# Performance work log

Measured on AMD Instinct MI355X. Metric: run time of the kernel, lower is better.

Reference implementation:

```python
import jax, jax.numpy as jnp
import numpy as np

D_MODEL = 1024
NUM_HEADS = 16
D_FF = 4096
BATCH = 4
SEQ = 1024
EPS = 1e-5
ROPE_THETA = 10000.0


def trunc_normal(key, shape):
    # approximate torch trunc_normal_(mean=0, std=1, a=-2, b=2)
    return jax.random.truncated_normal(key, -2.0, 2.0, shape, dtype=jnp.float32)


def setup_inputs() -> dict:
    key = jax.random.key(0)
    ks = jax.random.split(key, 10)
    d, h, f = D_MODEL, NUM_HEADS, D_FF
    return {
        "x": jax.random.normal(ks[0], (BATCH, SEQ, d), dtype=jnp.float32),
        "wq": trunc_normal(ks[1], (d, d)),
        "wk": trunc_normal(ks[2], (d, d)),
        "wv": trunc_normal(ks[3], (d, d)),
        "wo": trunc_normal(ks[4], (d, d)),
        "w1": trunc_normal(ks[5], (f, d)),
        "w2": trunc_normal(ks[6], (d, f)),
        "w3": trunc_normal(ks[7], (f, d)),
        "g1": trunc_normal(ks[8], (d,)),
        "g2": trunc_normal(ks[9], (d,)),
    }


def rms_norm(x, g):
    # source sums (x^2 + eps) then divides by d -> mean(x^2) + eps
    rms = jnp.sqrt(jnp.mean(jnp.square(x), axis=-1, keepdims=True) + EPS)
    return x * g / rms


def apply_rope(x, pos):
    # x: [b, h, s, d_k]; interleaved-pair rotation, theta=ROPE_THETA
    dk = x.shape[-1]
    inv_freq = ROPE_THETA ** (-jnp.arange(0, dk, 2, dtype=jnp.float32) / dk)
    ang = pos[:, None].astype(jnp.float32) * inv_freq[None, :]  # [s, dk/2]
    cos, sin = jnp.cos(ang), jnp.sin(ang)
    x1, x2 = x[..., 0::2], x[..., 1::2]
    r1 = x1 * cos - x2 * sin
    r2 = x1 * sin + x2 * cos
    return jnp.stack([r1, r2], axis=-1).reshape(x.shape)


def reference(x, wq, wk, wv, wo, w1, w2, w3, g1, g2):
    b, s, d = x.shape
    h, dk = NUM_HEADS, d // NUM_HEADS
    pos = jnp.arange(s)

    # --- attention sub-block (pre-norm) ---
    y = rms_norm(x, g1)
    q = (y @ wq.T).reshape(b, s, h, dk).transpose(0, 2, 1, 3)
    k = (y @ wk.T).reshape(b, s, h, dk).transpose(0, 2, 1, 3)
    v = (y @ wv.T).reshape(b, s, h, dk).transpose(0, 2, 1, 3)
    q = apply_rope(q, pos)
    k = apply_rope(k, pos)
    scores = jnp.einsum('bhqd,bhkd->bhqk', q, k) / jnp.sqrt(jnp.float32(dk))
    causal = jnp.tril(jnp.ones((s, s), dtype=bool))
    scores = jnp.where(causal, scores, -jnp.inf)
    attn = jax.nn.softmax(scores, axis=-1)
    ctx = jnp.einsum('bhqk,bhkd->bhqd', attn, v)
    ctx = ctx.transpose(0, 2, 1, 3).reshape(b, s, d)
    x = x + ctx @ wo.T

    # --- SwiGLU FFN sub-block (pre-norm) ---
    y = rms_norm(x, g2)
    l1 = y @ w1.T
    glu = (jax.nn.sigmoid(l1) * l1) * (y @ w3.T)
    return x + glu @ w2.T
```

## Files before the change

### kernel.cpp

```cpp
#include <hip/hip_runtime.h>

typedef __bf16 bf16;
typedef __attribute__((ext_vector_type(8))) __bf16 bf16x8;
typedef __attribute__((ext_vector_type(4))) float f32x4;

static __device__ __forceinline__ int swz4(int r) { return (r >> 1) & 3; }

static __device__ __forceinline__ void async_cp16(void* lds, const void* g) {
  __builtin_amdgcn_global_load_lds((__attribute__((address_space(1))) void*)g,
                                   (__attribute__((address_space(3))) void*)lds,
                                   16, 0, 0);
}

static __device__ __forceinline__ f32x4 mfma16(bf16x8 a, bf16x8 b, f32x4 c) {
  return __builtin_amdgcn_mfma_f32_16x16x32_bf16(a, b, c, 0, 0, 0);
}

static __device__ __forceinline__ unsigned short bfbits(float f) {
  bf16 b = (bf16)f;
  return __builtin_bit_cast(unsigned short, b);
}

extern "C" __global__ void prep_kernel(
    const float* __restrict__ wq, const float* __restrict__ wk,
    const float* __restrict__ wv, const float* __restrict__ wo,
    const float* __restrict__ w1, const float* __restrict__ w3,
    const float* __restrict__ w2,
    unsigned short* __restrict__ WQH, unsigned short* __restrict__ WQL,
    unsigned short* __restrict__ WKH, unsigned short* __restrict__ WKL,
    unsigned short* __restrict__ WVH, unsigned short* __restrict__ WOH,
    unsigned short* __restrict__ W1H, unsigned short* __restrict__ W3H,
    unsigned short* __restrict__ W2H, float2* __restrict__ rope) {
  const int seg = blockIdx.y;
  const int i = blockIdx.x * 256 + threadIdx.x;
  if (seg == 7) {
    if (i >= 32768) return;
    int s = i >> 5, fi = i & 31;
    float inv_freq = powf(10000.0f, -(2.0f * (float)fi) / 64.0f);
    float ang = (float)s * inv_freq;
    float2 cs;
    cs.x = cosf(ang);
    cs.y = sinf(ang);
    rope[i] = cs;
    return;
  }
  const float* src;
  unsigned short* hi_;
  unsigned short* lo_ = nullptr;
  int n4;
  switch (seg) {
    case 0: src = wq; hi_ = WQH; lo_ = WQL; n4 = 262144; break;
    case 1: src = wk; hi_ = WKH; lo_ = WKL; n4 = 262144; break;
    case 2: src = wv; hi_ = WVH; n4 = 262144; break;
    case 3: src = wo; hi_ = WOH; n4 = 262144; break;
    case 4: src = w1; hi_ = W1H; n4 = 1048576; break;
    case 5: src = w3; hi_ = W3H; n4 = 1048576; break;
    default: src = w2; hi_ = W2H; n4 = 1048576; break;
  }
  if (i >= n4) return;
  float4 v = ((const float4*)src)[i];
  bf16 b0 = (bf16)v.x, b1 = (bf16)v.y, b2 = (bf16)v.z, b3 = (bf16)v.w;
  ushort4 oh;
  oh.x = __builtin_bit_cast(unsigned short, b0);
  oh.y = __builtin_bit_cast(unsigned short, b1);
  oh.z = __builtin_bit_cast(unsigned short, b2);
  oh.w = __builtin_bit_cast(unsigned short, b3);
  ((ushort4*)hi_)[i] = oh;
  if (lo_) {
    ushort4 ol;
    ol.x = bfbits(v.x - (float)b0);
    ol.y = bfbits(v.y - (float)b1);
    ol.z = bfbits(v.z - (float)b2);
    ol.w = bfbits(v.w - (float)b3);
    ((ushort4*)lo_)[i] = ol;
  }
}

extern "C" __global__ __launch_bounds__(256) void rmsnorm_kernel(
    const float* __restrict__ x, const float* __restrict__ g,
    unsigned short* __restrict__ yhi, unsigned short* __restrict__ ylo) {
  int row = blockIdx.x;
  int t = threadIdx.x;
  const float4 xv = *(const float4*)(x + (size_t)row * 1024 + t * 4);
  float ss = xv.x * xv.x + xv.y * xv.y + xv.z * xv.z + xv.w * xv.w;
#pragma unroll
  for (int d = 1; d < 64; d <<= 1) ss += __shfl_xor(ss, d, 64);
  __shared__ float red[4];
  if ((t & 63) == 0) red[t >> 6] = ss;
  __syncthreads();
  float tot = red[0] + red[1] + red[2] + red[3];
  float inv = 1.0f / sqrtf(tot * (1.0f / 1024.0f) + 1e-5f);
  const float4 gv = *(const float4*)(g + t * 4);
  float y0 = xv.x * gv.x * inv, y1 = xv.y * gv.y * inv;
  float y2 = xv.z * gv.z * inv, y3 = xv.w * gv.w * inv;
  bf16 b0 = (bf16)y0, b1 = (bf16)y1, b2 = (bf16)y2, b3 = (bf16)y3;
  ushort4 oh;
  oh.x = __builtin_bit_cast(unsigned short, b0);
  oh.y = __builtin_bit_cast(unsigned short, b1);
  oh.z = __builtin_bit_cast(unsigned short, b2);
  oh.w = __builtin_bit_cast(unsigned short, b3);
  ((ushort4*)yhi)[(size_t)row * 256 + t] = oh;
  if (ylo) {
    ushort4 ol;
    ol.x = bfbits(y0 - (float)b0);
    ol.y = bfbits(y1 - (float)b1);
    ol.z = bfbits(y2 - (float)b2);
    ol.w = bfbits(y3 - (float)b3);
    ((ushort4*)ylo)[(size_t)row * 256 + t] = ol;
  }
}

template <int EPI>
__global__ __launch_bounds__(256, 2) void gemm_nt(
    const bf16* __restrict__ A, const bf16* __restrict__ B, int N, int K, int ldk,
    float* __restrict__ outF, bf16* __restrict__ outB,
    const float* __restrict__ resF) {
  const int bid = blockIdx.x;
  const int xcd = bid & 7, sq = bid >> 3;
  const int z = sq >> 5;
  const int rem = sq & 31;
  const size_t tm = (size_t)(xcd * 4 + (rem >> 3)) * 128;
  const size_t tn = (size_t)(rem & 7) * 128;
  A += (size_t)z * K;
  B += (size_t)z * K;
  __shared__ alignas(16) bf16 As[128 * 64];
  __shared__ alignas(16) bf16 Bs[128 * 64];
  const int tid = threadIdx.x;
  const int lane = tid & 63, wave = tid >> 6;
  const int lo = lane & 15, hi = lane >> 4;
  const int wm = wave >> 1, wn = wave & 1;
  f32x4 acc[4][4] = {};
  for (int k0 = 0; k0 < K; k0 += 64) {
    __syncthreads();
#pragma unroll
    for (int i4 = 0; i4 < 4; i4++) {
      int p = tid + 256 * i4;
      int row = p >> 3, c = p & 7;
      int cs = c ^ (row & 7);
      async_cp16((char*)As + (size_t)p * 16, A + (tm + row) * (size_t)ldk + k0 + cs * 8);
      async_cp16((char*)Bs + (size_t)p * 16, B + (tn + row) * (size_t)ldk + k0 + cs * 8);
    }
    __syncthreads();
#pragma unroll
    for (int kh = 0; kh < 2; kh++) {
      bf16x8 fa[4], fb[4];
#pragma unroll
      for (int i = 0; i < 4; i++) {
        int ra = wm * 64 + i * 16 + lo;
        fa[i] = *(const bf16x8*)((const char*)As + ra * 128 + (((kh * 4 + hi) ^ (ra & 7)) << 4));
        int rb = wn * 64 + i * 16 + lo;
        fb[i] = *(const bf16x8*)((const char*)Bs + rb * 128 + (((kh * 4 + hi) ^ (rb & 7)) << 4));
      }
      __builtin_amdgcn_s_setprio(1);
#pragma unroll
      for (int i = 0; i < 4; i++)
#pragma unroll
        for (int j = 0; j < 4; j++) acc[i][j] = mfma16(fa[i], fb[j], acc[i][j]);
      __builtin_amdgcn_s_setprio(0);
    }
  }
#pragma unroll
  for (int i = 0; i < 4; i++)
#pragma unroll
    for (int j = 0; j < 4; j++)
#pragma unroll
      for (int r = 0; r < 4; r++) {
        size_t m = tm + wm * 64 + i * 16 + hi * 4 + r;
        size_t n = tn + wn * 64 + j * 16 + lo;
        float v = acc[i][j][r];
        if constexpr (EPI == 1) {
          size_t idx = m * (size_t)N + n;
          outF[idx] = v + resF[idx];
        } else {
          atomicAdd(&outF[m * (size_t)N + n], v);
        }
      }
}

extern "C" __global__ __launch_bounds__(256, 2) void gemm_up_kernel(
    const bf16* __restrict__ A, const bf16* __restrict__ B1,
    const bf16* __restrict__ B3, bf16* __restrict__ G) {
  const int bid = blockIdx.x;
  const int xcd = bid & 7, sq = bid >> 3;
  const size_t tm = (size_t)(xcd * 4 + (sq & 3)) * 128;
  const size_t tn = (size_t)(sq >> 2) * 128;
  __shared__ alignas(16) bf16 As[128 * 64];
  __shared__ alignas(16) bf16 B1s[128 * 64];
  __shared__ alignas(16) bf16 B3s[128 * 64];
  const int tid = threadIdx.x;
  const int lane = tid & 63, wave = tid >> 6;
  const int lo = lane & 15, hi = lane >> 4;
  const int wm = wave >> 1, wn = wave & 1;
  f32x4 acc1[4][4] = {}, acc3[4][4] = {};
  for (int k0 = 0; k0 < 1024; k0 += 64) {
    __syncthreads();
#pragma unroll
    for (int i4 = 0; i4 < 4; i4++) {
      int p = tid + 256 * i4;
      int row = p >> 3, c = p & 7;
      int cs = c ^ (row & 7);
      async_cp16((char*)As + (size_t)p * 16, A + (tm + row) * (size_t)1024 + k0 + cs * 8);
      async_cp16((char*)B1s + (size_t)p * 16, B1 + (tn + row) * (size_t)1024 + k0 + cs * 8);
      async_cp16((char*)B3s + (size_t)p * 16, B3 + (tn + row) * (size_t)1024 + k0 + cs * 8);
    }
    __syncthreads();
#pragma unroll
    for (int kh = 0; kh < 2; kh++) {
      bf16x8 fa[4], fb[4];
#pragma unroll
      for (int i = 0; i < 4; i++) {
        int ra = wm * 64 + i * 16 + lo;
        fa[i] = *(const bf16x8*)((const char*)As + ra * 128 + (((kh * 4 + hi) ^ (ra & 7)) << 4));
        int rb = wn * 64 + i * 16 + lo;
        fb[i] = *(const bf16x8*)((const char*)B1s + rb * 128 + (((kh * 4 + hi) ^ (rb & 7)) << 4));
      }
      __builtin_amdgcn_s_setprio(1);
#pragma unroll
      for (int i = 0; i < 4; i++)
#pragma unroll
        for (int j = 0; j < 4; j++) acc1[i][j] = mfma16(fa[i], fb[j], acc1[i][j]);
      __builtin_amdgcn_s_setprio(0);
#pragma unroll
      for (int j = 0; j < 4; j++) {
        int rb = wn * 64 + j * 16 + lo;
        fb[j] = *(const bf16x8*)((const char*)B3s + rb * 128 + (((kh * 4 + hi) ^ (rb & 7)) << 4));
      }
      __builtin_amdgcn_s_setprio(1);
#pragma unroll
      for (int i = 0; i < 4; i++)
#pragma unroll
        for (int j = 0; j < 4; j++) acc3[i][j] = mfma16(fa[i], fb[j], acc3[i][j]);
      __builtin_amdgcn_s_setprio(0);
    }
  }
#pragma unroll
  for (int i = 0; i < 4; i++)
#pragma unroll
    for (int j = 0; j < 4; j++)
#pragma unroll
      for (int r = 0; r < 4; r++) {
        size_t m = tm + wm * 64 + i * 16 + hi * 4 + r;
        size_t n = tn + wn * 64 + j * 16 + lo;
        float v1 = acc1[i][j][r], v3 = acc3[i][j][r];
        G[m * 4096 + n] = (bf16)(v1 / (1.0f + __expf(-v1)) * v3);
      }
}

extern "C" __global__ __launch_bounds__(256, 2) void gemm_qkv_kernel(
    const bf16* __restrict__ Ah, const bf16* __restrict__ Al,
    const bf16* __restrict__ BhQ, const bf16* __restrict__ BlQ,
    const bf16* __restrict__ BhK, const bf16* __restrict__ BlK,
    const bf16* __restrict__ BV,
    const float2* __restrict__ rope,
    bf16* __restrict__ OhQ, bf16* __restrict__ OlQ,
    bf16* __restrict__ OhK, bf16* __restrict__ OlK,
    bf16* __restrict__ Vt) {
  const int bid = blockIdx.x;
  const int xcd = bid & 7, sq = bid >> 3;
  const int z = sq >> 5;
  const int rem = sq & 31;
  const size_t tm = (size_t)(xcd * 4 + (rem >> 3)) * 128;
  const size_t tn = (size_t)(rem & 7) * 128;
  const bf16* Bh = (z == 0) ? BhQ : (z == 1) ? BhK : BV;
  const bf16* Bl = (z == 1) ? BlK : BlQ;
  __shared__ alignas(16) bf16 Ahs[128 * 64], Als[128 * 64];
  __shared__ alignas(16) bf16 Bhs[128 * 64], Bls[128 * 64];
  const int tid = threadIdx.x;
  const int lane = tid & 63, wave = tid >> 6;
  const int lo = lane & 15, hi = lane >> 4;
  const int wm = wave >> 1, wn = wave & 1;
  const int K = 1024;
  f32x4 acc[4][4] = {};
  for (int k0 = 0; k0 < K; k0 += 64) {
    __syncthreads();
#pragma unroll
    for (int i4 = 0; i4 < 4; i4++) {
      int p = tid + 256 * i4;
      int row = p >> 3, c = p & 7;
      int cs = c ^ (row & 7);
      size_t ga = (tm + row) * (size_t)K + k0 + cs * 8;
      size_t gb = (tn + row) * (size_t)K + k0 + cs * 8;
      async_cp16((char*)Ahs + (size_t)p * 16, Ah + ga);
      async_cp16((char*)Bhs + (size_t)p * 16, Bh + gb);
      if (z < 2) {
        async_cp16((char*)Als + (size_t)p * 16, Al + ga);
        async_cp16((char*)Bls + (size_t)p * 16, Bl + gb);
      }
    }
    __syncthreads();
#pragma unroll
    for (int kh = 0; kh < 2; kh++) {
      int offa[4], offb[4];
#pragma unroll
      for (int i = 0; i < 4; i++) {
        int ra = wm * 64 + i * 16 + lo;
        offa[i] = ra * 128 + (((kh * 4 + hi) ^ (ra & 7)) << 4);
        int rb = wn * 64 + i * 16 + lo;
        offb[i] = rb * 128 + (((kh * 4 + hi) ^ (rb & 7)) << 4);
      }
      bf16x8 fah[4], fbh[4], fx[4];
#pragma unroll
      for (int i = 0; i < 4; i++) {
        fah[i] = *(const bf16x8*)((const char*)Ahs + offa[i]);
        fbh[i] = *(const bf16x8*)((const char*)Bhs + offb[i]);
      }
      __builtin_amdgcn_s_setprio(1);
#pragma unroll
      for (int i = 0; i < 4; i++)
#pragma unroll
        for (int j = 0; j < 4; j++) acc[i][j] = mfma16(fah[i], fbh[j], acc[i][j]);
      __builtin_amdgcn_s_setprio(0);
      if (z < 2) {
#pragma unroll
        for (int j = 0; j < 4; j++) fx[j] = *(const bf16x8*)((const char*)Bls + offb[j]);
        __builtin_amdgcn_s_setprio(1);
#pragma unroll
        for (int i = 0; i < 4; i++)
#pragma unroll
          for (int j = 0; j < 4; j++) acc[i][j] = mfma16(fah[i], fx[j], acc[i][j]);
        __builtin_amdgcn_s_setprio(0);
#pragma unroll
        for (int i = 0; i < 4; i++) fx[i] = *(const bf16x8*)((const char*)Als + offa[i]);
        __builtin_amdgcn_s_setprio(1);
#pragma unroll
        for (int i = 0; i < 4; i++)
#pragma unroll
          for (int j = 0; j < 4; j++) acc[i][j] = mfma16(fx[i], fbh[j], acc[i][j]);
        __builtin_amdgcn_s_setprio(0);
      }
    }
  }
  if (z < 2) {
    bf16* Oh = z ? OhK : OhQ;
    bf16* Ol = z ? OlK : OlQ;
#pragma unroll
    for (int i = 0; i < 4; i++)
#pragma unroll
      for (int j = 0; j < 4; j++)
#pragma unroll
        for (int r = 0; r < 4; r++) {
          float v = acc[i][j][r];
          float vp = __shfl_xor(v, 1, 64);
          size_t m = tm + wm * 64 + i * 16 + hi * 4 + r;
          size_t n = tn + wn * 64 + j * 16 + lo;
          int s = (int)(m & 1023);
          int pi = (int)((n & 63) >> 1);
          float2 cs = rope[s * 32 + pi];
          float res = (n & 1) ? (vp * cs.y + v * cs.x) : (v * cs.x - vp * cs.y);
          size_t idx = (((m >> 10) * 16 + (n >> 6)) * 1024 + (m & 1023)) * 64 + (n & 63);
          bf16 hb = (bf16)res;
          Oh[idx] = hb;
          Ol[idx] = (bf16)(res - (float)hb);
        }
  } else {
#pragma unroll
    for (int i = 0; i < 4; i++)
#pragma unroll
      for (int j = 0; j < 4; j++)
#pragma unroll
        for (int r = 0; r < 4; r++) {
          size_t m = tm + wm * 64 + i * 16 + hi * 4 + r;
          size_t n = tn + wn * 64 + j * 16 + lo;
          size_t idx = (((m >> 10) * 16 + (n >> 6)) * 64 + (n & 63)) * 1024 + (m & 1023);
          Vt[idx] = (bf16)acc[i][j][r];
        }
  }
}

extern "C" __global__ __launch_bounds__(256, 4) void flash_kernel(
    const bf16* __restrict__ qhi, const bf16* __restrict__ qlo,
    const bf16* __restrict__ khi, const bf16* __restrict__ klo,
    const bf16* __restrict__ vT, bf16* __restrict__ ctx) {
  const int bid = blockIdx.x;
  const int qb = bid >> 6;
  const int bh = bid & 63;
  const int tid = threadIdx.x;
  const int wave = tid >> 6, lane = tid & 63;
  const int lo = lane & 15, hi = lane >> 4;

  __shared__ alignas(16) bf16 Ksh[2][64][32];
  __shared__ alignas(16) bf16 Ksl[2][64][32];
  __shared__ alignas(16) bf16 Vs[2][64][32];
  __shared__ alignas(16) bf16 P[4][16][72];

  size_t qoff = ((size_t)bh * 1024 + qb * 64 + wave * 16 + lo) * 64;
  bf16x8 qh[2], ql[2];
#pragma unroll
  for (int ks = 0; ks < 2; ks++) {
    qh[ks] = *(const bf16x8*)(qhi + qoff + ks * 32 + hi * 8);
    ql[ks] = *(const bf16x8*)(qlo + qoff + ks * 32 + hi * 8);
  }

  const int srow = tid >> 2;
  const int scl = (tid & 3) ^ swz4(srow);
  const size_t kgb = (size_t)bh * 1024 * 64;
  const size_t vgb = ((size_t)bh * 64 + srow) * 1024;

  float mrun[4] = {-1e30f, -1e30f, -1e30f, -1e30f};
  float lrun[4] = {0.f, 0.f, 0.f, 0.f};
  f32x4 o[4] = {};
  const float scale = 0.125f;

  for (int kt = 0; kt <= qb; kt++) {
    __syncthreads();
#pragma unroll
    for (int i = 0; i < 2; i++) {
      int p = tid + 256 * i;
      size_t gk = kgb + (size_t)(kt * 64 + srow) * 64 + i * 32 + scl * 8;
      async_cp16((char*)Ksh + (size_t)p * 16, khi + gk);
      async_cp16((char*)Ksl + (size_t)p * 16, klo + gk);
      async_cp16((char*)Vs + (size_t)p * 16, vT + vgb + kt * 64 + i * 32 + scl * 8);
    }
    __syncthreads();

    f32x4 sv[4];
    __builtin_amdgcn_s_setprio(1);
#pragma unroll
    for (int nb = 0; nb < 4; nb++) {
      f32x4 a = {0.f, 0.f, 0.f, 0.f};
#pragma unroll
      for (int ks = 0; ks < 2; ks++) {
        int row = nb * 16 + lo;
        int off16 = (ks * 64 + row) * 4 + (hi ^ swz4(row));
        bf16x8 kh = *(const bf16x8*)((const char*)Ksh + off16 * 16);
        bf16x8 kl = *(const bf16x8*)((const char*)Ksl + off16 * 16);
        a = mfma16(qh[ks], kh, a);
        a = mfma16(qh[ks], kl, a);
        a = mfma16(ql[ks], kh, a);
      }
      sv[nb] = a;
    }
    __builtin_amdgcn_s_setprio(0);

    const bool mt = (kt == qb);
#pragma unroll
    for (int nb = 0; nb < 4; nb++)
#pragma unroll
      for (int r = 0; r < 4; r++) {
        float s = sv[nb][r] * scale;
        if (mt) {
          int kp = nb * 16 + lo;
          int qr = wave * 16 + hi * 4 + r;
          if (kp > qr) s = -1e30f;
        }
        sv[nb][r] = s;
      }
    float mnew[4], rs[4];
#pragma unroll
    for (int r = 0; r < 4; r++) {
      float mx = fmaxf(fmaxf(sv[0][r], sv[1][r]), fmaxf(sv[2][r], sv[3][r]));
#pragma unroll
      for (int d = 1; d < 16; d <<= 1) mx = fmaxf(mx, __shfl_xor(mx, d, 64));
      mnew[r] = fmaxf(mrun[r], mx);
      float sc = __expf(mrun[r] - mnew[r]);
      lrun[r] *= sc;
#pragma unroll
      for (int db = 0; db < 4; db++) o[db][r] *= sc;
      mrun[r] = mnew[r];
      rs[r] = 0.f;
    }
#pragma unroll
    for (int nb = 0; nb < 4; nb++)
#pragma unroll
      for (int r = 0; r < 4; r++) {
        float p = __expf(sv[nb][r] - mnew[r]);
        bf16 pb = (bf16)p;
        rs[r] += (float)pb;
        P[wave][hi * 4 + r][nb * 16 + lo] = pb;
      }
#pragma unroll
    for (int r = 0; r < 4; r++) {
      float t = rs[r];
#pragma unroll
      for (int d = 1; d < 16; d <<= 1) t += __shfl_xor(t, d, 64);
      lrun[r] += t;
    }
    bf16x8 pa[2];
#pragma unroll
    for (int ks = 0; ks < 2; ks++) pa[ks] = *(const bf16x8*)&P[wave][lo][ks * 32 + hi * 8];
    __builtin_amdgcn_s_setprio(1);
#pragma unroll
    for (int db = 0; db < 4; db++)
#pragma unroll
      for (int ks = 0; ks < 2; ks++) {
        int row = db * 16 + lo;
        int off16 = (ks * 64 + row) * 4 + (hi ^ swz4(row));
        bf16x8 vf = *(const bf16x8*)((const char*)Vs + off16 * 16);
        o[db] = mfma16(pa[ks], vf, o[db]);
      }
    __builtin_amdgcn_s_setprio(0);
  }
  int b = bh >> 4, h = bh & 15;
#pragma unroll
  for (int db = 0; db < 4; db++)
#pragma unroll
    for (int r = 0; r < 4; r++) {
      float val = o[db][r] / lrun[r];
      size_t row = (size_t)b * 1024 + qb * 64 + wave * 16 + hi * 4 + r;
      ctx[row * 1024 + h * 64 + db * 16 + lo] = (bf16)val;
    }
}


extern "C" void kernel_launch(void* const* d_in, const int* in_sizes, int n_in,
                              void* d_out, int out_size, void* d_ws, size_t ws_size,
                              hipStream_t stream) {
  (void)in_sizes; (void)n_in; (void)out_size; (void)ws_size;
  const float* x  = (const float*)d_in[0];
  const float* wq = (const float*)d_in[1];
  const float* wk = (const float*)d_in[2];
  const float* wv = (const float*)d_in[3];
  const float* wo = (const float*)d_in[4];
  const float* w1 = (const float*)d_in[5];
  const float* w2 = (const float*)d_in[6];
  const float* w3 = (const float*)d_in[7];
  const float* g1 = (const float*)d_in[8];
  const float* g2 = (const float*)d_in[9];
  float* out = (float*)d_out;

  char* ws = (char*)d_ws;
  size_t off = 0;
  auto alloc = [&](size_t bytes) {
    char* p = ws + off;
    off += (bytes + 255) & ~(size_t)255;
    return p;
  };
  const size_t MB2 = 1024u * 1024u * 2u;
  const size_t MB8 = 4096u * 1024u * 2u;
  void* WQH = alloc(MB2);  void* WQL = alloc(MB2);
  void* WKH = alloc(MB2);  void* WKL = alloc(MB2);
  void* WVH = alloc(MB2);  void* WOH = alloc(MB2);
  void* W1H = alloc(MB8);  void* W3H = alloc(MB8);  void* W2H = alloc(MB8);
  void* ROPE = alloc(32768u * 8u);
  void* Y1H = alloc(MB8);  void* Y1L = alloc(MB8);
  void* QH = alloc(MB8);   void* QL = alloc(MB8);
  void* KH = alloc(MB8);   void* KL = alloc(MB8);
  void* VT = alloc(MB8);
  void* CTX = alloc(MB8);
  void* Y2H = alloc(MB8);
  void* GLU = QH;

  prep_kernel<<<dim3(4096, 8), dim3(256), 0, stream>>>(
      wq, wk, wv, wo, w1, w3, w2,
      (unsigned short*)WQH, (unsigned short*)WQL, (unsigned short*)WKH,
      (unsigned short*)WKL, (unsigned short*)WVH, (unsigned short*)WOH,
      (unsigned short*)W1H, (unsigned short*)W3H, (unsigned short*)W2H,
      (float2*)ROPE);

  rmsnorm_kernel<<<dim3(4096), dim3(256), 0, stream>>>(
      x, g1, (unsigned short*)Y1H, (unsigned short*)Y1L);

  gemm_qkv_kernel<<<dim3(768), dim3(256), 0, stream>>>(
      (const bf16*)Y1H, (const bf16*)Y1L,
      (const bf16*)WQH, (const bf16*)WQL, (const bf16*)WKH, (const bf16*)WKL,
      (const bf16*)WVH,
      (const float2*)ROPE,
      (bf16*)QH, (bf16*)QL, (bf16*)KH, (bf16*)KL, (bf16*)VT);

  flash_kernel<<<dim3(1024), dim3(256), 0, stream>>>(
      (const bf16*)QH, (const bf16*)QL, (const bf16*)KH, (const bf16*)KL,
      (const bf16*)VT, (bf16*)CTX);

  gemm_nt<1><<<dim3(256), dim3(256), 0, stream>>>(
      (const bf16*)CTX, (const bf16*)WOH, 1024, 1024, 1024,
      out, nullptr, x);

  rmsnorm_kernel<<<dim3(4096), dim3(256), 0, stream>>>(
      out, g2, (unsigned short*)Y2H, nullptr);

  gemm_up_kernel<<<dim3(1024), dim3(256), 0, stream>>>(
      (const bf16*)Y2H, (const bf16*)W1H, (const bf16*)W3H, (bf16*)GLU);

  gemm_nt<5><<<dim3(512), dim3(256), 0, stream>>>(
      (const bf16*)GLU, (const bf16*)W2H, 1024, 2048, 4096,
      out, nullptr, nullptr);
}
```

Measured before the change: 285.4 us.

## Split-K output projection with atomics; copy residual in rmsnorm; interleave QKV tiles

The first rmsnorm now also writes x into the output buffer. This lets the output projection run as a split-K GEMM (two K halves, 512 blocks) that atomically adds into out, instead of a 256-block GEMM that adds the residual in its epilogue. The QKV GEMM block mapping now interleaves the Q/K/V selector across consecutive blocks, so each XCD works on all three projections of the same A tile. The aim is better CU occupancy for the small output GEMM and better cache reuse of A. In exchange the output GEMM pays for atomic adds, and the copy adds one extra full write of x.

```diff
diff --git a/kernel.cpp b/kernel.cpp
--- a/kernel.cpp
+++ b/kernel.cpp
@@ -78,7 +78,8 @@
 
 extern "C" __global__ __launch_bounds__(256) void rmsnorm_kernel(
     const float* __restrict__ x, const float* __restrict__ g,
-    unsigned short* __restrict__ yhi, unsigned short* __restrict__ ylo) {
+    unsigned short* __restrict__ yhi, unsigned short* __restrict__ ylo,
+    float* __restrict__ xcopy) {
   int row = blockIdx.x;
   int t = threadIdx.x;
   const float4 xv = *(const float4*)(x + (size_t)row * 1024 + t * 4);
@@ -108,13 +109,13 @@
     ol.w = bfbits(y3 - (float)b3);
     ((ushort4*)ylo)[(size_t)row * 256 + t] = ol;
   }
+  if (xcopy) *(float4*)(xcopy + (size_t)row * 1024 + t * 4) = xv;
 }
 
 template <int EPI>
 __global__ __launch_bounds__(256, 2) void gemm_nt(
     const bf16* __restrict__ A, const bf16* __restrict__ B, int N, int K, int ldk,
-    float* __restrict__ outF, bf16* __restrict__ outB,
-    const float* __restrict__ resF) {
+    float* __restrict__ outF) {
   const int bid = blockIdx.x;
   const int xcd = bid & 7, sq = bid >> 3;
   const int z = sq >> 5;
@@ -167,13 +168,7 @@
       for (int r = 0; r < 4; r++) {
         size_t m = tm + wm * 64 + i * 16 + hi * 4 + r;
         size_t n = tn + wn * 64 + j * 16 + lo;
-        float v = acc[i][j][r];
-        if constexpr (EPI == 1) {
-          size_t idx = m * (size_t)N + n;
-          outF[idx] = v + resF[idx];
-        } else {
-          atomicAdd(&outF[m * (size_t)N + n], v);
-        }
+        atomicAdd(&outF[m * (size_t)N + n], acc[i][j][r]);
       }
 }
 
@@ -257,10 +252,10 @@
     bf16* __restrict__ Vt) {
   const int bid = blockIdx.x;
   const int xcd = bid & 7, sq = bid >> 3;
-  const int z = sq >> 5;
-  const int rem = sq & 31;
-  const size_t tm = (size_t)(xcd * 4 + (rem >> 3)) * 128;
-  const size_t tn = (size_t)(rem & 7) * 128;
+  const int z = sq % 3;
+  const int t = sq / 3;
+  const size_t tm = (size_t)(xcd * 4 + (t >> 3)) * 128;
+  const size_t tn = (size_t)(t & 7) * 128;
   const bf16* Bh = (z == 0) ? BhQ : (z == 1) ? BhK : BV;
   const bf16* Bl = (z == 1) ? BlK : BlQ;
   __shared__ alignas(16) bf16 Ahs[128 * 64], Als[128 * 64];
@@ -548,7 +543,7 @@
       (float2*)ROPE);
 
   rmsnorm_kernel<<<dim3(4096), dim3(256), 0, stream>>>(
-      x, g1, (unsigned short*)Y1H, (unsigned short*)Y1L);
+      x, g1, (unsigned short*)Y1H, (unsigned short*)Y1L, out);
 
   gemm_qkv_kernel<<<dim3(768), dim3(256), 0, stream>>>(
       (const bf16*)Y1H, (const bf16*)Y1L,
@@ -561,17 +556,15 @@
       (const bf16*)QH, (const bf16*)QL, (const bf16*)KH, (const bf16*)KL,
       (const bf16*)VT, (bf16*)CTX);
 
-  gemm_nt<1><<<dim3(256), dim3(256), 0, stream>>>(
-      (const bf16*)CTX, (const bf16*)WOH, 1024, 1024, 1024,
-      out, nullptr, x);
+  gemm_nt<5><<<dim3(512), dim3(256), 0, stream>>>(
+      (const bf16*)CTX, (const bf16*)WOH, 1024, 512, 1024, out);
 
   rmsnorm_kernel<<<dim3(4096), dim3(256), 0, stream>>>(
-      out, g2, (unsigned short*)Y2H, nullptr);
+      out, g2, (unsigned short*)Y2H, nullptr, nullptr);
 
   gemm_up_kernel<<<dim3(1024), dim3(256), 0, stream>>>(
       (const bf16*)Y2H, (const bf16*)W1H, (const bf16*)W3H, (bf16*)GLU);
 
   gemm_nt<5><<<dim3(512), dim3(256), 0, stream>>>(
-      (const bf16*)GLU, (const bf16*)W2H, 1024, 2048, 4096,
-      out, nullptr, nullptr);
-}
+      (const bf16*)GLU, (const bf16*)W2H, 1024, 2048, 4096, out);
+}
```

After: 313.3 us. 9.7% more time.
